# Kernel tuning notes

Hardware: AMD Instinct MI355X
Metric: run time of the kernel (lower is better)

The kernel has to match this reference:

```python
import jax, jax.numpy as jnp
import numpy as np
from jax import lax

B, DIM, H, W = 8, 192, 128, 128
K = 7            # kernel_size
STRIDE = 1
PAD = 3          # kernel_size // 2
RED = 4          # reduction
HID = DIM // RED # 48
EPS = 1e-5       # BatchNorm eps


def setup_inputs() -> dict:
    key = jax.random.key(0)
    ks = jax.random.split(key, 4)
    return {
        "x": jax.random.normal(ks[0], (B, DIM, H, W), dtype=jnp.float32),
        # conv1: 1x1, no bias -> [out=HID, in=DIM]
        "w1": jax.random.normal(ks[1], (HID, DIM), dtype=jnp.float32) * 0.05,
        # BatchNorm2d(HID) eval-mode params / running stats
        "bn_gamma": jnp.ones((HID,), jnp.float32),
        "bn_beta": jnp.zeros((HID,), jnp.float32),
        "bn_mean": jnp.zeros((HID,), jnp.float32),
        "bn_var": jnp.ones((HID,), jnp.float32),
        # conv2: 1x1 -> [out=DIM*K*K, in=HID], with bias
        "w2": jax.random.normal(ks[2], (DIM * K * K, HID), dtype=jnp.float32) * 0.05,
        "b2": jnp.zeros((DIM * K * K,), jnp.float32),
        # depthwise output bias (self.bias)
        "bias": jax.random.normal(ks[3], (DIM,), dtype=jnp.float32) * 0.05,
    }


def reference(x, w1, bn_gamma, bn_beta, bn_mean, bn_var, w2, b2, bias):
    b, c, h, w = x.shape
    # SE-style weight generation: pool -> 1x1 conv -> BN -> ReLU -> 1x1 conv
    pooled = x.mean(axis=(2, 3))                          # [b, c]
    y = jnp.einsum('bc,oc->bo', pooled, w1)               # [b, HID]
    y = (y - bn_mean) * lax.rsqrt(bn_var + EPS) * bn_gamma + bn_beta
    y = jax.nn.relu(y)
    wdyn = jnp.einsum('bh,oh->bo', y, w2) + b2            # [b, c*K*K]
    wdyn = wdyn.reshape(b, c, K, K)                       # per-sample depthwise kernels

    # per-sample depthwise conv (equiv. to groups=b*dim batch-folded trick)
    def dw(xi, wi):  # xi: [c,h,w], wi: [c,K,K]
        return lax.conv_general_dilated(
            xi[None], wi[:, None],              # [1,c,h,w], [c,1,K,K] (OIHW)
            window_strides=(STRIDE, STRIDE),
            padding=[(PAD, PAD), (PAD, PAD)],
            feature_group_count=c)[0]

    out = jax.vmap(dw)(x, wdyn) + bias[None, :, None, None]
    return out
```

## Files before the change

kernel.cpp:

```cpp
#include <hip/hip_runtime.h>

#define BATCH 8
#define DIM 192
#define HH 128
#define WW 128
#define KS 7
#define PAD 3
#define HID 48
#define KK 49
#define BN_EPS 1e-5f

#define TILE_H 32
#define SROWS (TILE_H + KS - 1)
#define NSLOT (SROWS * (WW / 4))
#define NTILE (HH / TILE_H)
#define RPT   4

static_assert(NSLOT % 64 == 0, "staging guard must be wave-uniform");

__global__ __launch_bounds__(256) void pool_kernel(const float* __restrict__ x,
                                                   float* __restrict__ pooled) {
    const int bc = blockIdx.x;
    const float4* p = (const float4*)(x + (size_t)bc * HH * WW);
    const int t = threadIdx.x;
    float s = 0.f;
#pragma unroll
    for (int i = 0; i < 16; ++i) {
        float4 v = p[t + i * 256];
        s += (v.x + v.y) + (v.z + v.w);
    }
#pragma unroll
    for (int off = 32; off > 0; off >>= 1) s += __shfl_down(s, off, 64);
    __shared__ float wsum[4];
    const int wave = t >> 6, lane = t & 63;
    if (lane == 0) wsum[wave] = s;
    __syncthreads();
    if (t == 0) {
        float tot = (wsum[0] + wsum[1]) + (wsum[2] + wsum[3]);
        pooled[bc] = tot * (1.0f / (HH * WW));
    }
}

__global__ __launch_bounds__(256) void dwconv_fused_kernel(
        const float* __restrict__ x,
        const float* __restrict__ pooled,
        const float* __restrict__ w1,
        const float* __restrict__ gamma,
        const float* __restrict__ beta,
        const float* __restrict__ mean,
        const float* __restrict__ var,
        const float* __restrict__ w2,
        const float* __restrict__ b2,
        const float* __restrict__ bias,
        float* __restrict__ out) {
    __shared__ float smem[SROWS][WW];
    __shared__ float y_s[HID];
    __shared__ float wk_s[KK];
    const int tile = blockIdx.x & (NTILE - 1);
    const int bc = blockIdx.x >> 2;
    const int b = bc / DIM;
    const int c = bc % DIM;
    const int t = threadIdx.x;
    const int r0 = tile * TILE_H;

    const int slo = (tile == 0) ? PAD * (WW / 4) : 0;
    const int shi = (tile == NTILE - 1) ? (SROWS - PAD) * (WW / 4) : NSLOT;
    const float* xbase = x + (size_t)bc * HH * WW + (ptrdiff_t)(r0 - PAD) * WW;

#pragma unroll
    for (int i = 0; i < (NSLOT + 255) / 256; ++i) {
        const int s = t + i * 256;
        if (s < NSLOT) {
            int sc = s;
            if (sc < slo) sc = slo;
            if (sc >= shi) sc = shi - 1;
            __builtin_amdgcn_global_load_lds(
                (const __attribute__((address_space(1))) void*)(xbase + (size_t)sc * 4),
                (__attribute__((address_space(3))) void*)((float*)smem + (size_t)s * 4),
                16, 0, 0);
        }
    }

    if (t < HID) {
        const float4* pr = (const float4*)(pooled + b * DIM);
        const float4* wr = (const float4*)(w1 + (size_t)t * DIM);
        float acc = 0.f;
#pragma unroll
        for (int j = 0; j < DIM / 4; ++j) {
            float4 pv = pr[j], wv = wr[j];
            acc += pv.x * wv.x + pv.y * wv.y + pv.z * wv.z + pv.w * wv.w;
        }
        float yv = (acc - mean[t]) * rsqrtf(var[t] + BN_EPS) * gamma[t] + beta[t];
        y_s[t] = yv > 0.f ? yv : 0.f;
    }
    __syncthreads();

    if (t < KK) {
        const int o = c * KK + t;
        const float4* w2r = (const float4*)(w2 + (size_t)o * HID);
        float acc = b2[o];
#pragma unroll
        for (int j = 0; j < HID / 4; ++j) {
            float4 wv = w2r[j];
            acc += y_s[4 * j] * wv.x + y_s[4 * j + 1] * wv.y +
                   y_s[4 * j + 2] * wv.z + y_s[4 * j + 3] * wv.w;
        }
        wk_s[t] = acc;
    } else if (t >= 160) {
        const int zi = t - 160;
        if (tile == 0) {
            ((float4*)smem)[zi] = make_float4(0.f, 0.f, 0.f, 0.f);
        } else if (tile == NTILE - 1) {
            ((float4*)smem)[(SROWS - PAD) * (WW / 4) + zi] =
                make_float4(0.f, 0.f, 0.f, 0.f);
        }
    }
    __syncthreads();

    float wreg[KK];
#pragma unroll
    for (int i = 0; i < KK; ++i) wreg[i] = wk_s[i];
    const float bv = bias[c];

    const int c4 = t & 31;
    const int strip = t >> 5;
    const int sbase = strip * RPT;
    float* outp = out + (size_t)bc * HH * WW + (size_t)(r0 + sbase) * WW + c4 * 4;

    float acc[RPT][4];
#pragma unroll
    for (int i = 0; i < RPT; ++i)
        acc[i][0] = acc[i][1] = acc[i][2] = acc[i][3] = 0.f;

#pragma unroll
    for (int ir = 0; ir < RPT + KS - 1; ++ir) {
        const float4* row4 = (const float4*)&smem[sbase + ir][0];
        const float4 f1 = row4[c4];
        float4 f0 = make_float4(0.f, 0.f, 0.f, 0.f);
        float4 f2 = make_float4(0.f, 0.f, 0.f, 0.f);
        if (c4 > 0)  f0 = row4[c4 - 1];
        if (c4 < 31) f2 = row4[c4 + 1];
        const float v[12] = {f0.x, f0.y, f0.z, f0.w,
                             f1.x, f1.y, f1.z, f1.w,
                             f2.x, f2.y, f2.z, f2.w};
#pragma unroll
        for (int ky = 0; ky < KS; ++ky) {
            const int o = ir - ky;
            if (o >= 0 && o < RPT) {
                float* a = acc[o];
#pragma unroll
                for (int kx = 0; kx < KS; ++kx) {
                    const float wv = wreg[ky * KS + kx];
                    a[0] += wv * v[1 + kx];
                    a[1] += wv * v[2 + kx];
                    a[2] += wv * v[3 + kx];
                    a[3] += wv * v[4 + kx];
                }
            }
        }
        if (ir >= KS - 1) {
            float* a = acc[ir - (KS - 1)];
            float4 o4 = make_float4(a[0] + bv, a[1] + bv, a[2] + bv, a[3] + bv);
            *((float4*)(outp + (size_t)(ir - (KS - 1)) * WW)) = o4;
        }
    }
}

extern "C" void kernel_launch(void* const* d_in, const int* in_sizes, int n_in,
                              void* d_out, int out_size, void* d_ws, size_t ws_size,
                              hipStream_t stream) {
    const float* x     = (const float*)d_in[0];
    const float* w1    = (const float*)d_in[1];
    const float* gamma = (const float*)d_in[2];
    const float* beta  = (const float*)d_in[3];
    const float* mean  = (const float*)d_in[4];
    const float* var   = (const float*)d_in[5];
    const float* w2    = (const float*)d_in[6];
    const float* b2    = (const float*)d_in[7];
    const float* bias  = (const float*)d_in[8];
    float* out = (float*)d_out;

    float* pooled = (float*)d_ws;

    pool_kernel<<<BATCH * DIM, 256, 0, stream>>>(x, pooled);
    dwconv_fused_kernel<<<BATCH * DIM * NTILE, 256, 0, stream>>>(
        x, pooled, w1, gamma, beta, mean, var, w2, b2, bias, out);
}
```

Before: 258.1 us.

## Process all row tiles per block with double-buffered LDS staging

Each block now handles one whole (batch, channel) plane and loops over the four row tiles. The next tile is loaded into a second LDS buffer while the current tile is computed. This amortises the per-block dynamic-weight generation (the w1 and w2 matvecs) across four tiles instead of redoing it per tile, and hides global-load latency. The cost is a quarter as many blocks (1536 instead of 6144) and doubled LDS per block, which lowers occupancy and parallelism. Correctness relies on the load-to-LDS being complete at the barrier after each tile.

Measured after the change: 257.6 us. About the same (-0.2%).

```diff
diff --git a/kernel.cpp b/kernel.cpp
--- a/kernel.cpp
+++ b/kernel.cpp
@@ -53,33 +53,36 @@
         const float* __restrict__ b2,
         const float* __restrict__ bias,
         float* __restrict__ out) {
-    __shared__ float smem[SROWS][WW];
+    __shared__ float smem[2][SROWS][WW];
     __shared__ float y_s[HID];
     __shared__ float wk_s[KK];
-    const int tile = blockIdx.x & (NTILE - 1);
-    const int bc = blockIdx.x >> 2;
+    const int bc = blockIdx.x;
     const int b = bc / DIM;
     const int c = bc % DIM;
     const int t = threadIdx.x;
-    const int r0 = tile * TILE_H;
-
-    const int slo = (tile == 0) ? PAD * (WW / 4) : 0;
-    const int shi = (tile == NTILE - 1) ? (SROWS - PAD) * (WW / 4) : NSLOT;
-    const float* xbase = x + (size_t)bc * HH * WW + (ptrdiff_t)(r0 - PAD) * WW;
-
-#pragma unroll
-    for (int i = 0; i < (NSLOT + 255) / 256; ++i) {
-        const int s = t + i * 256;
-        if (s < NSLOT) {
-            int sc = s;
-            if (sc < slo) sc = slo;
-            if (sc >= shi) sc = shi - 1;
-            __builtin_amdgcn_global_load_lds(
-                (const __attribute__((address_space(1))) void*)(xbase + (size_t)sc * 4),
-                (__attribute__((address_space(3))) void*)((float*)smem + (size_t)s * 4),
-                16, 0, 0);
-        }
-    }
+    const float* xchan = x + (size_t)bc * HH * WW;
+
+    auto stage = [&](int tile, int bufi) {
+        const int slo = (tile == 0) ? PAD * (WW / 4) : 0;
+        const int shi = (tile == NTILE - 1) ? (SROWS - PAD) * (WW / 4) : NSLOT;
+        const float* xbase = xchan + (ptrdiff_t)(tile * TILE_H - PAD) * WW;
+        float* dst = &smem[bufi][0][0];
+#pragma unroll
+        for (int i = 0; i < (NSLOT + 255) / 256; ++i) {
+            const int s = t + i * 256;
+            if (s < NSLOT) {
+                int sc = s;
+                if (sc < slo) sc = slo;
+                if (sc >= shi) sc = shi - 1;
+                __builtin_amdgcn_global_load_lds(
+                    (const __attribute__((address_space(1))) void*)(xbase + (size_t)sc * 4),
+                    (__attribute__((address_space(3))) void*)(dst + (size_t)s * 4),
+                    16, 0, 0);
+            }
+        }
+    };
+
+    stage(0, 0);
 
     if (t < HID) {
         const float4* pr = (const float4*)(pooled + b * DIM);
@@ -108,12 +111,7 @@
         wk_s[t] = acc;
     } else if (t >= 160) {
         const int zi = t - 160;
-        if (tile == 0) {
-            ((float4*)smem)[zi] = make_float4(0.f, 0.f, 0.f, 0.f);
-        } else if (tile == NTILE - 1) {
-            ((float4*)smem)[(SROWS - PAD) * (WW / 4) + zi] =
-                make_float4(0.f, 0.f, 0.f, 0.f);
-        }
+        ((float4*)&smem[0][0][0])[zi] = make_float4(0.f, 0.f, 0.f, 0.f);
     }
     __syncthreads();
 
@@ -125,43 +123,60 @@
     const int c4 = t & 31;
     const int strip = t >> 5;
     const int sbase = strip * RPT;
-    float* outp = out + (size_t)bc * HH * WW + (size_t)(r0 + sbase) * WW + c4 * 4;
-
-    float acc[RPT][4];
-#pragma unroll
-    for (int i = 0; i < RPT; ++i)
-        acc[i][0] = acc[i][1] = acc[i][2] = acc[i][3] = 0.f;
-
-#pragma unroll
-    for (int ir = 0; ir < RPT + KS - 1; ++ir) {
-        const float4* row4 = (const float4*)&smem[sbase + ir][0];
-        const float4 f1 = row4[c4];
-        float4 f0 = make_float4(0.f, 0.f, 0.f, 0.f);
-        float4 f2 = make_float4(0.f, 0.f, 0.f, 0.f);
-        if (c4 > 0)  f0 = row4[c4 - 1];
-        if (c4 < 31) f2 = row4[c4 + 1];
-        const float v[12] = {f0.x, f0.y, f0.z, f0.w,
-                             f1.x, f1.y, f1.z, f1.w,
-                             f2.x, f2.y, f2.z, f2.w};
-#pragma unroll
-        for (int ky = 0; ky < KS; ++ky) {
-            const int o = ir - ky;
-            if (o >= 0 && o < RPT) {
-                float* a = acc[o];
-#pragma unroll
-                for (int kx = 0; kx < KS; ++kx) {
-                    const float wv = wreg[ky * KS + kx];
-                    a[0] += wv * v[1 + kx];
-                    a[1] += wv * v[2 + kx];
-                    a[2] += wv * v[3 + kx];
-                    a[3] += wv * v[4 + kx];
+
+#pragma unroll 1
+    for (int tile = 0; tile < NTILE; ++tile) {
+        const int cur = tile & 1;
+        if (tile + 1 < NTILE) stage(tile + 1, cur ^ 1);
+
+        float* outp = out + (size_t)bc * HH * WW +
+                      (size_t)(tile * TILE_H + sbase) * WW + c4 * 4;
+        float acc[RPT][4];
+#pragma unroll
+        for (int i = 0; i < RPT; ++i)
+            acc[i][0] = acc[i][1] = acc[i][2] = acc[i][3] = 0.f;
+
+#pragma unroll
+        for (int ir = 0; ir < RPT + KS - 1; ++ir) {
+            const float4* row4 = (const float4*)&smem[cur][sbase + ir][0];
+            const float4 f1 = row4[c4];
+            float4 f0 = make_float4(0.f, 0.f, 0.f, 0.f);
+            float4 f2 = make_float4(0.f, 0.f, 0.f, 0.f);
+            if (c4 > 0)  f0 = row4[c4 - 1];
+            if (c4 < 31) f2 = row4[c4 + 1];
+            const float v[12] = {f0.x, f0.y, f0.z, f0.w,
+                                 f1.x, f1.y, f1.z, f1.w,
+                                 f2.x, f2.y, f2.z, f2.w};
+#pragma unroll
+            for (int ky = 0; ky < KS; ++ky) {
+                const int o = ir - ky;
+                if (o >= 0 && o < RPT) {
+                    float* a = acc[o];
+#pragma unroll
+                    for (int kx = 0; kx < KS; ++kx) {
+                        const float wv = wreg[ky * KS + kx];
+                        a[0] += wv * v[1 + kx];
+                        a[1] += wv * v[2 + kx];
+                        a[2] += wv * v[3 + kx];
+                        a[3] += wv * v[4 + kx];
+                    }
                 }
             }
-        }
-        if (ir >= KS - 1) {
-            float* a = acc[ir - (KS - 1)];
-            float4 o4 = make_float4(a[0] + bv, a[1] + bv, a[2] + bv, a[3] + bv);
-            *((float4*)(outp + (size_t)(ir - (KS - 1)) * WW)) = o4;
+            if (ir >= KS - 1) {
+                float* a = acc[ir - (KS - 1)];
+                float4 o4 = make_float4(a[0] + bv, a[1] + bv, a[2] + bv, a[3] + bv);
+                *((float4*)(outp + (size_t)(ir - (KS - 1)) * WW)) = o4;
+            }
+        }
+
+        if (tile + 1 < NTILE) {
+            __syncthreads();
+            if (tile + 1 == NTILE - 1) {
+                if (t < 96)
+                    ((float4*)&smem[1][0][0])[(SROWS - PAD) * (WW / 4) + t] =
+                        make_float4(0.f, 0.f, 0.f, 0.f);
+                __syncthreads();
+            }
         }
     }
 }
@@ -183,6 +198,6 @@
     float* pooled = (float*)d_ws;
 
     pool_kernel<<<BATCH * DIM, 256, 0, stream>>>(x, pooled);
-    dwconv_fused_kernel<<<BATCH * DIM * NTILE, 256, 0, stream>>>(
+    dwconv_fused_kernel<<<BATCH * DIM, 256, 0, stream>>>(
         x, pooled, w1, gamma, beta, mean, var, w2, b2, bias, out);
 }
```

## Hoist dynamic weight generation into separate kernel and double conv tile height

Applied to the files above, without the earlier changes.

Moves the SE-style weight generation (pool→FC→BN→ReLU→FC) out of the depthwise conv kernel into its own small kernel, so each conv block only loads 49 precomputed weights instead of recomputing the MLP for every tile. It also doubles the tile height to 64 rows with 8 output rows per thread, using a rolling 7-entry accumulator ring, which cuts halo overhead and redundant per-tile work. The cost is an extra kernel launch, a workspace round trip, larger shared memory per block and fewer blocks, which may reduce occupancy.

New measurement: 226.2 us. -12.4%, faster.

```diff
diff --git a/kernel.cpp b/kernel.cpp
--- a/kernel.cpp
+++ b/kernel.cpp
@@ -9,12 +9,13 @@
 #define HID 48
 #define KK 49
 #define BN_EPS 1e-5f
+#define WSTR 52
 
-#define TILE_H 32
+#define TILE_H 64
 #define SROWS (TILE_H + KS - 1)
 #define NSLOT (SROWS * (WW / 4))
 #define NTILE (HH / TILE_H)
-#define RPT   4
+#define RPT   8
 
 static_assert(NSLOT % 64 == 0, "staging guard must be wave-uniform");
 
@@ -41,8 +42,7 @@
     }
 }
 
-__global__ __launch_bounds__(256) void dwconv_fused_kernel(
-        const float* __restrict__ x,
+__global__ __launch_bounds__(64) void wgen_full_kernel(
         const float* __restrict__ pooled,
         const float* __restrict__ w1,
         const float* __restrict__ gamma,
@@ -51,14 +51,47 @@
         const float* __restrict__ var,
         const float* __restrict__ w2,
         const float* __restrict__ b2,
+        float* __restrict__ wdyn) {
+    __shared__ float y_s[HID];
+    const int bc = blockIdx.x;
+    const int b = bc / DIM, c = bc % DIM;
+    const int t = threadIdx.x;
+    if (t < HID) {
+        const float4* pr = (const float4*)(pooled + b * DIM);
+        const float4* wr = (const float4*)(w1 + (size_t)t * DIM);
+        float acc = 0.f;
+#pragma unroll
+        for (int j = 0; j < DIM / 4; ++j) {
+            float4 pv = pr[j], wv = wr[j];
+            acc += pv.x * wv.x + pv.y * wv.y + pv.z * wv.z + pv.w * wv.w;
+        }
+        float yv = (acc - mean[t]) * rsqrtf(var[t] + BN_EPS) * gamma[t] + beta[t];
+        y_s[t] = yv > 0.f ? yv : 0.f;
+    }
+    __syncthreads();
+    if (t < KK) {
+        const int o = c * KK + t;
+        const float4* w2r = (const float4*)(w2 + (size_t)o * HID);
+        float acc = b2[o];
+#pragma unroll
+        for (int j = 0; j < HID / 4; ++j) {
+            float4 wv = w2r[j];
+            acc += y_s[4 * j] * wv.x + y_s[4 * j + 1] * wv.y +
+                   y_s[4 * j + 2] * wv.z + y_s[4 * j + 3] * wv.w;
+        }
+        wdyn[(size_t)bc * WSTR + t] = acc;
+    }
+}
+
+__global__ __launch_bounds__(256) void dwconv_hoisted_kernel(
+        const float* __restrict__ x,
+        const float* __restrict__ wdyn,
         const float* __restrict__ bias,
         float* __restrict__ out) {
     __shared__ float smem[SROWS][WW];
-    __shared__ float y_s[HID];
     __shared__ float wk_s[KK];
     const int tile = blockIdx.x & (NTILE - 1);
-    const int bc = blockIdx.x >> 2;
-    const int b = bc / DIM;
+    const int bc = blockIdx.x >> 1;
     const int c = bc % DIM;
     const int t = threadIdx.x;
     const int r0 = tile * TILE_H;
@@ -81,39 +114,12 @@
         }
     }
 
-    if (t < HID) {
-        const float4* pr = (const float4*)(pooled + b * DIM);
-        const float4* wr = (const float4*)(w1 + (size_t)t * DIM);
-        float acc = 0.f;
-#pragma unroll
-        for (int j = 0; j < DIM / 4; ++j) {
-            float4 pv = pr[j], wv = wr[j];
-            acc += pv.x * wv.x + pv.y * wv.y + pv.z * wv.z + pv.w * wv.w;
-        }
-        float yv = (acc - mean[t]) * rsqrtf(var[t] + BN_EPS) * gamma[t] + beta[t];
-        y_s[t] = yv > 0.f ? yv : 0.f;
-    }
+    if (t < KK) wk_s[t] = wdyn[(size_t)bc * WSTR + t];
     __syncthreads();
 
-    if (t < KK) {
-        const int o = c * KK + t;
-        const float4* w2r = (const float4*)(w2 + (size_t)o * HID);
-        float acc = b2[o];
-#pragma unroll
-        for (int j = 0; j < HID / 4; ++j) {
-            float4 wv = w2r[j];
-            acc += y_s[4 * j] * wv.x + y_s[4 * j + 1] * wv.y +
-                   y_s[4 * j + 2] * wv.z + y_s[4 * j + 3] * wv.w;
-        }
-        wk_s[t] = acc;
-    } else if (t >= 160) {
-        const int zi = t - 160;
-        if (tile == 0) {
-            ((float4*)smem)[zi] = make_float4(0.f, 0.f, 0.f, 0.f);
-        } else if (tile == NTILE - 1) {
-            ((float4*)smem)[(SROWS - PAD) * (WW / 4) + zi] =
-                make_float4(0.f, 0.f, 0.f, 0.f);
-        }
+    if (t < 96) {
+        const int zslot = (tile ? (SROWS - PAD) * (WW / 4) : 0) + t;
+        ((float4*)smem)[zslot] = make_float4(0.f, 0.f, 0.f, 0.f);
     }
     __syncthreads();
 
@@ -127,9 +133,9 @@
     const int sbase = strip * RPT;
     float* outp = out + (size_t)bc * HH * WW + (size_t)(r0 + sbase) * WW + c4 * 4;
 
-    float acc[RPT][4];
+    float acc[7][4];
 #pragma unroll
-    for (int i = 0; i < RPT; ++i)
+    for (int i = 0; i < 7; ++i)
         acc[i][0] = acc[i][1] = acc[i][2] = acc[i][3] = 0.f;
 
 #pragma unroll
@@ -147,7 +153,7 @@
         for (int ky = 0; ky < KS; ++ky) {
             const int o = ir - ky;
             if (o >= 0 && o < RPT) {
-                float* a = acc[o];
+                float* a = acc[o % 7];
 #pragma unroll
                 for (int kx = 0; kx < KS; ++kx) {
                     const float wv = wreg[ky * KS + kx];
@@ -159,9 +165,10 @@
             }
         }
         if (ir >= KS - 1) {
-            float* a = acc[ir - (KS - 1)];
+            float* a = acc[(ir - (KS - 1)) % 7];
             float4 o4 = make_float4(a[0] + bv, a[1] + bv, a[2] + bv, a[3] + bv);
             *((float4*)(outp + (size_t)(ir - (KS - 1)) * WW)) = o4;
+            a[0] = a[1] = a[2] = a[3] = 0.f;
         }
     }
 }
@@ -181,8 +188,11 @@
     float* out = (float*)d_out;
 
     float* pooled = (float*)d_ws;
+    float* wdyn   = pooled + BATCH * DIM;
 
     pool_kernel<<<BATCH * DIM, 256, 0, stream>>>(x, pooled);
-    dwconv_fused_kernel<<<BATCH * DIM * NTILE, 256, 0, stream>>>(
-        x, pooled, w1, gamma, beta, mean, var, w2, b2, bias, out);
+    wgen_full_kernel<<<BATCH * DIM, 64, 0, stream>>>(
+        pooled, w1, gamma, beta, mean, var, w2, b2, wdyn);
+    dwconv_hoisted_kernel<<<BATCH * DIM * NTILE, 256, 0, stream>>>(
+        x, wdyn, bias, out);
 }
```
